# Optimization experiments

Hardware: AMD Instinct MI355X
Metric: run time of the kernel (lower is better)

The kernel has to match this reference:

```python
import jax, jax.numpy as jnp
import numpy as np

B, T, L, D, H = 8, 4, 512, 512, 8
HD = D // H
THR = 1.0
BETA = 0.5
EPS = 1e-5


def heaviside(x):
    return (x >= 0).astype(x.dtype)


def bn_eval(x, g, b, rm, rv):
    # BatchNorm1d in eval mode applied on the last dim
    return (x - rm) * (g * jax.lax.rsqrt(rv + EPS)) + b


def lif(x_btld):
    # snntorch Leaky(beta=0.5, threshold=1, reset='subtract'), mem init 0, scan over T
    xs = jnp.moveaxis(x_btld, 1, 0)  # (T,B,L,D)

    def step(mem, xt):
        reset = heaviside(mem - THR)          # reset from previous mem (detached in torch)
        mem = BETA * mem + xt - reset * THR
        spk = heaviside(mem - THR)
        return mem, spk

    _, spks = jax.lax.scan(step, jnp.zeros_like(xs[0]), xs)
    return jnp.moveaxis(spks, 0, 1)


def setup_inputs() -> dict:
    key = jax.random.key(0)
    ks = jax.random.split(key, 24)
    s = D ** -0.5
    inp = {
        "x": jax.random.normal(ks[0], (B, T, L, D), jnp.float32),
        "q_w": jax.random.normal(ks[1], (D, D), jnp.float32) * s,
        "q_g": jax.random.normal(ks[2], (D,), jnp.float32),
        "q_b": jax.random.normal(ks[3], (D,), jnp.float32),
        "q_rm": jax.random.normal(ks[4], (D,), jnp.float32),
        "q_rv": jax.random.uniform(ks[5], (D,), jnp.float32),
        "k_w": jax.random.normal(ks[6], (D, D), jnp.float32) * s,
        "k_g": jax.random.normal(ks[7], (D,), jnp.float32),
        "k_b": jax.random.normal(ks[8], (D,), jnp.float32),
        "k_rm": jax.random.normal(ks[9], (D,), jnp.float32),
        "k_rv": jax.random.uniform(ks[10], (D,), jnp.float32),
        "v_w": jax.random.normal(ks[11], (D, D), jnp.float32) * s,
        "v_g": jax.random.normal(ks[12], (D,), jnp.float32),
        "v_b": jax.random.normal(ks[13], (D,), jnp.float32),
        "v_rm": jax.random.normal(ks[14], (D,), jnp.float32),
        "v_rv": jax.random.uniform(ks[15], (D,), jnp.float32),
        "o_w": jax.random.normal(ks[16], (D, D), jnp.float32) * s,
        "o_bias": jax.random.normal(ks[17], (D,), jnp.float32),
        "o_g": jax.random.normal(ks[18], (D,), jnp.float32),
        "o_b": jax.random.normal(ks[19], (D,), jnp.float32),
        "o_rm": jax.random.normal(ks[20], (D,), jnp.float32),
        "o_rv": jax.random.uniform(ks[21], (D,), jnp.float32),
    }
    return inp


def reference(x, q_w, q_g, q_b, q_rm, q_rv, k_w, k_g, k_b, k_rm, k_rv,
              v_w, v_g, v_b, v_rm, v_rv, o_w, o_bias, o_g, o_b, o_rm, o_rv):
    scale = HD ** -0.5
    # Q path: linear -> BN -> LIF (binary {0,1})
    q = bn_eval(jnp.einsum('btld,ed->btle', x, q_w), q_g, q_b, q_rm, q_rv)
    q = lif(q)
    # K path: linear -> BN -> ReLU (continuous)
    k = jax.nn.relu(bn_eval(jnp.einsum('btld,ed->btle', x, k_w), k_g, k_b, k_rm, k_rv))
    # V path: linear -> BN -> ternary {-1,0,+1}
    v = bn_eval(jnp.einsum('btld,ed->btle', x, v_w), v_g, v_b, v_rm, v_rv)
    v = heaviside(v - THR) - heaviside(-v - THR)
    # split heads: (B,T,H,L,hd)
    sh = lambda a: a.reshape(B, T, L, H, HD).transpose(0, 1, 3, 2, 4)
    q, k, v = sh(q), sh(k), sh(v)
    attn = jnp.einsum('bthld,bthmd->bthlm', q, k) * scale
    out = jnp.einsum('bthlm,bthmd->bthld', attn, v)
    out = out.transpose(0, 1, 3, 2, 4).reshape(B, T, L, D)
    out = jnp.einsum('btld,ed->btle', out, o_w) + o_bias
    out = bn_eval(out, o_g, o_b, o_rm, o_rv)
    return lif(out)
```

## Files before the change

kernel.cpp:

```cpp
#include <hip/hip_runtime.h>
#include <math.h>
#include <stdint.h>

#define Bb 8
#define Tt 4
#define Ll 512
#define Dd 512
#define Hh 8
#define HDd 64
#define Mm (Bb*Tt*Ll)

typedef _Float16 f16;
typedef _Float16 f16x8 __attribute__((ext_vector_type(8)));
typedef _Float16 f16x4 __attribute__((ext_vector_type(4)));
typedef float f32x4 __attribute__((ext_vector_type(4)));

#define LO_SCALE 2048.0f
#define LO_INV   4.8828125e-4f

__device__ __forceinline__ void gload16(const void* g, void* l) {
  __builtin_amdgcn_global_load_lds(
      (const __attribute__((address_space(1))) unsigned int*)(uintptr_t)g,
      (__attribute__((address_space(3))) unsigned int*)(uintptr_t)l,
      16, 0, 0);
}

struct SplitArgs {
  const float* src[5];
  f16* hi[5];
  f16* lo[5];
};

__global__ void split_k(SplitArgs s) {
  int i = blockIdx.x * 256 + threadIdx.x;
  int seg, base;
  if (i < 1048576) { seg = 0; base = i; }
  else { int r = i - 1048576; seg = 1 + (r >> 15); base = r & 32767; }
  const float* sp = s.src[seg] + (size_t)base * 8;
  float4 v0 = *(const float4*)sp;
  float4 v1 = *(const float4*)(sp + 4);
  float a[8] = {v0.x, v0.y, v0.z, v0.w, v1.x, v1.y, v1.z, v1.w};
  f16x8 hv, lv;
  #pragma unroll
  for (int e = 0; e < 8; ++e) {
    f16 hh = (f16)a[e];
    hv[e] = hh;
    lv[e] = (f16)((a[e] - (float)hh) * LO_SCALE);
  }
  *(f16x8*)(s.hi[seg] + (size_t)base * 8) = hv;
  *(f16x8*)(s.lo[seg] + (size_t)base * 8) = lv;
}

struct GArgs {
  const f16 *Ah, *Al;
  const f16 *Wh0, *Wl0, *Wh1, *Wl1, *Wh2, *Wl2;
  const float *g0,*b0,*rm0,*rv0;
  const float *g1,*b1,*rm1,*rv1;
  const float *g2,*b2,*rm2,*rv2;
  const float* bias;
  f16*   oq;
  float* ok;
  f16*   ov;
  float* oo;
};

#define SMEM_BYTES 34048

template<int MODE>
__global__ __launch_bounds__(256, 2)
void gemm_f16(GArgs ar) {
  extern __shared__ __align__(16) char smem[];
  f16* Ah_s = (f16*)smem;
  f16* Al_s = (f16*)(smem + 8192);
  f16* Bh_s = (f16*)(smem + 16384);
  f16* Bl_s = (f16*)(smem + 24576);
  float (*TS)[133] = (float(*)[133])smem;

  const int tid = threadIdx.x;
  const int lane = tid & 63, wid = tid >> 6;
  const int bx = blockIdx.x, by = blockIdx.y;
  const int seg = (MODE == 0) ? (bx >> 2) : 0;
  const int lc0 = (MODE == 0) ? ((bx & 3) << 7) : (bx << 7);
  const int b = by >> 4, lc32 = by & 15;

  const f16* Wh = (seg == 0 ? ar.Wh0 : (seg == 1 ? ar.Wh1 : ar.Wh2));
  const f16* Wl = (seg == 0 ? ar.Wl0 : (seg == 1 ? ar.Wl1 : ar.Wl2));
  const float* gp  = (seg == 0 ? ar.g0  : (seg == 1 ? ar.g1  : ar.g2));
  const float* bp  = (seg == 0 ? ar.b0  : (seg == 1 ? ar.b1  : ar.b2));
  const float* rmp = (seg == 0 ? ar.rm0 : (seg == 1 ? ar.rm1 : ar.rm2));
  const float* rvp = (seg == 0 ? ar.rv0 : (seg == 1 ? ar.rv1 : ar.rv2));

  const int srow = lane >> 2, skc = lane & 3;
  const int fr = lane & 15, kg = lane >> 4;
  const int wmr = wid >> 1, wnc = wid & 1;

  f32x4 acc_h[4][4], acc_l[4][4];
  #pragma unroll
  for (int i = 0; i < 4; ++i)
    #pragma unroll
    for (int j = 0; j < 4; ++j) {
      acc_h[i][j] = (f32x4)0.0f;
      acc_l[i][j] = (f32x4)0.0f;
    }

  for (int k0 = 0; k0 < Dd; k0 += 32) {
    __syncthreads();
    #pragma unroll
    for (int i = 0; i < 2; ++i) {
      const int r = i * 64 + wid * 16 + srow;
      const int grow = (((b << 2) + (r >> 5)) << 9) + (lc32 << 5) + (r & 31);
      const size_t goA = (size_t)grow * Dd + k0 + skc * 8;
      const size_t goB = (size_t)(lc0 + r) * Dd + k0 + skc * 8;
      const int lbase = i * 2048 + wid * 512;
      gload16(ar.Ah + goA, Ah_s + lbase);
      gload16(ar.Al + goA, Al_s + lbase);
      gload16(Wh + goB, Bh_s + lbase);
      gload16(Wl + goB, Bl_s + lbase);
    }
    __syncthreads();

    f16x8 a_h[4], a_l[4], b_h[4], b_l[4];
    #pragma unroll
    for (int i = 0; i < 4; ++i) {
      const int ra = (wmr * 64 + i * 16 + fr) * 32 + kg * 8;
      a_h[i] = *(const f16x8*)&Ah_s[ra];
      a_l[i] = *(const f16x8*)&Al_s[ra];
      const int rb = (wnc * 64 + i * 16 + fr) * 32 + kg * 8;
      b_h[i] = *(const f16x8*)&Bh_s[rb];
      b_l[i] = *(const f16x8*)&Bl_s[rb];
    }
    #pragma unroll
    for (int i = 0; i < 4; ++i)
      #pragma unroll
      for (int j = 0; j < 4; ++j) {
        acc_h[i][j] = __builtin_amdgcn_mfma_f32_16x16x32_f16(a_h[i], b_h[j], acc_h[i][j], 0, 0, 0);
        acc_l[i][j] = __builtin_amdgcn_mfma_f32_16x16x32_f16(a_h[i], b_l[j], acc_l[i][j], 0, 0, 0);
        acc_l[i][j] = __builtin_amdgcn_mfma_f32_16x16x32_f16(a_l[i], b_h[j], acc_l[i][j], 0, 0, 0);
      }
  }

  float scl[4], shc[4];
  #pragma unroll
  for (int j = 0; j < 4; ++j) {
    const int c = lc0 + wnc * 64 + j * 16 + fr;
    double S = (double)gp[c] / sqrt((double)rvp[c] + 1e-5);
    double Sh = (double)bp[c] - (double)rmp[c] * S;
    if (MODE == 1) Sh += (double)ar.bias[c] * S;
    scl[j] = (float)S; shc[j] = (float)Sh;
  }

  if (MODE == 0 && seg != 0) {
    #pragma unroll
    for (int i = 0; i < 4; ++i)
      #pragma unroll
      for (int r = 0; r < 4; ++r) {
        const int tr = wmr * 64 + i * 16 + (kg << 2) + r;
        const int grow = (((b << 2) + (tr >> 5)) << 9) + (lc32 << 5) + (tr & 31);
        #pragma unroll
        for (int j = 0; j < 4; ++j) {
          const int col = lc0 + wnc * 64 + j * 16 + fr;
          float val = acc_h[i][j][r] + acc_l[i][j][r] * LO_INV;
          float y = val * scl[j] + shc[j];
          if (seg == 1) ar.ok[(size_t)grow * Dd + col] = fmaxf(y, 0.f);
          else ar.ov[(size_t)grow * Dd + col] =
                   (f16)((y >= 1.f ? 1.f : 0.f) - (-y >= 1.f ? 1.f : 0.f));
        }
      }
    return;
  }

  __syncthreads();
  #pragma unroll
  for (int half = 0; half < 2; ++half) {
    if (wnc == half) {
      #pragma unroll
      for (int i = 0; i < 4; ++i)
        #pragma unroll
        for (int j = 0; j < 4; ++j) {
          float4 yv;
          float* yp = &yv.x;
          #pragma unroll
          for (int r = 0; r < 4; ++r) {
            float val = acc_h[i][j][r] + acc_l[i][j][r] * LO_INV;
            yp[r] = val * scl[j] + shc[j];
          }
          *(float4*)&TS[j * 16 + fr][wmr * 64 + i * 16 + (kg << 2)] = yv;
        }
    }
    __syncthreads();
    const int cc4 = (tid & 15) << 2;
    #pragma unroll
    for (int rr = 0; rr < 2; ++rr) {
      const int rl = (tid >> 4) + (rr << 4);
      float mm[4] = {0.f, 0.f, 0.f, 0.f};
      #pragma unroll
      for (int t = 0; t < 4; ++t) {
        const int trow = t * 32 + rl;
        float sp[4];
        #pragma unroll
        for (int c = 0; c < 4; ++c) {
          float y = TS[cc4 + c][trow];
          float rst = (mm[c] >= 1.f) ? 1.f : 0.f;
          mm[c] = 0.5f * mm[c] + y - rst;
          sp[c] = (mm[c] >= 1.f) ? 1.f : 0.f;
        }
        const size_t go = ((size_t)((((b << 2) + t) << 9) + (lc32 << 5) + rl)) * Dd
                          + lc0 + (half << 6) + cc4;
        if (MODE == 0) {
          f16x4 s4;
          s4[0] = (f16)sp[0]; s4[1] = (f16)sp[1]; s4[2] = (f16)sp[2]; s4[3] = (f16)sp[3];
          *(f16x4*)(ar.oq + go) = s4;
        } else {
          *(float4*)(ar.oo + go) = make_float4(sp[0], sp[1], sp[2], sp[3]);
        }
      }
    }
    __syncthreads();
  }
}

__global__ __launch_bounds__(256)
void attn_g(const float* __restrict__ ks, const f16* __restrict__ vs,
            float* __restrict__ pG) {
  const int bt = blockIdx.x, h = blockIdx.y, c = blockIdx.z;
  const float* kp = ks + (size_t)bt * Ll * Dd + h * HDd;
  const f16* vp = vs + (size_t)bt * Ll * Dd + h * HDd;

  __shared__ float KS[64][68];
  __shared__ float VS[64][68];
  const int tid = threadIdx.x;
  const int te = tid & 15, td = tid >> 4;

  float gacc[4][4];
  #pragma unroll
  for (int i = 0; i < 4; ++i)
    #pragma unroll
    for (int j = 0; j < 4; ++j) gacc[i][j] = 0.f;

  for (int mt = 0; mt < 2; ++mt) {
    const int m0 = c * 128 + mt * 64;
    #pragma unroll
    for (int it = 0; it < 4; ++it) {
      int fidx = it * 256 + tid;
      int row = fidx >> 4, fq = fidx & 15;
      *(float4*)&KS[row][fq << 2] = *(const float4*)(kp + (size_t)(m0 + row) * Dd + (fq << 2));
    }
    #pragma unroll
    for (int it = 0; it < 2; ++it) {
      int fidx = it * 256 + tid;
      int row = fidx >> 3, c8 = fidx & 7;
      f16x8 hv = *(const f16x8*)(vp + (size_t)(m0 + row) * Dd + (c8 << 3));
      *(float4*)&VS[row][c8 << 3] = make_float4(hv[0], hv[1], hv[2], hv[3]);
      *(float4*)&VS[row][(c8 << 3) + 4] = make_float4(hv[4], hv[5], hv[6], hv[7]);
    }
    __syncthreads();
    #pragma unroll 4
    for (int mm = 0; mm < 64; ++mm) {
      float4 k4 = *(const float4*)&KS[mm][te << 2];
      float4 v4 = *(const float4*)&VS[mm][td << 2];
      const float kk[4] = {k4.x, k4.y, k4.z, k4.w};
      const float vv[4] = {v4.x, v4.y, v4.z, v4.w};
      #pragma unroll
      for (int i = 0; i < 4; ++i)
        #pragma unroll
        for (int j = 0; j < 4; ++j)
          gacc[i][j] = fmaf(kk[i], vv[j], gacc[i][j]);
    }
    __syncthreads();
  }
  float* out = pG + (((size_t)(bt * 8 + h) * 4 + c) << 12);
  #pragma unroll
  for (int i = 0; i < 4; ++i)
    *(float4*)&out[((te << 2) + i) * 64 + (td << 2)] =
        make_float4(gacc[i][0] * 0.125f, gacc[i][1] * 0.125f,
                    gacc[i][2] * 0.125f, gacc[i][3] * 0.125f);
}

__global__ __launch_bounds__(256)
void attn_o(const f16* __restrict__ qs, const float* __restrict__ pG,
            f16* __restrict__ ahi, f16* __restrict__ alo) {
  const int bt = blockIdx.x, h = blockIdx.y, lc = blockIdx.z;
  __shared__ float G[64][68];
  __shared__ float QS[64][68];
  const int tid = threadIdx.x;

  const float* pg = pG + (((size_t)(bt * 8 + h) * 4) << 12);
  #pragma unroll
  for (int rep = 0; rep < 4; ++rep) {
    int t4 = rep * 256 + tid;
    int e = t4 >> 4, dq = t4 & 15;
    int off = e * 64 + (dq << 2);
    float4 s0 = *(const float4*)(pg + off);
    float4 s1 = *(const float4*)(pg + 4096 + off);
    float4 s2 = *(const float4*)(pg + 8192 + off);
    float4 s3 = *(const float4*)(pg + 12288 + off);
    *(float4*)&G[e][dq << 2] = make_float4(s0.x + s1.x + s2.x + s3.x,
                                           s0.y + s1.y + s2.y + s3.y,
                                           s0.z + s1.z + s2.z + s3.z,
                                           s0.w + s1.w + s2.w + s3.w);
  }
  __syncthreads();

  const f16* qp = qs + (size_t)bt * Ll * Dd + h * HDd;
  const int lr = tid >> 2, dg = tid & 3;

  for (int l0 = 0; l0 < 128; l0 += 64) {
    #pragma unroll
    for (int it = 0; it < 2; ++it) {
      int fidx = it * 256 + tid;
      int row = fidx >> 3, c8 = fidx & 7;
      f16x8 hv = *(const f16x8*)(qp + (size_t)(lc * 128 + l0 + row) * Dd + (c8 << 3));
      *(float4*)&QS[row][c8 << 3] = make_float4(hv[0], hv[1], hv[2], hv[3]);
      *(float4*)&QS[row][(c8 << 3) + 4] = make_float4(hv[4], hv[5], hv[6], hv[7]);
    }
    __syncthreads();
    float oacc[16];
    #pragma unroll
    for (int j = 0; j < 16; ++j) oacc[j] = 0.f;
    for (int ee = 0; ee < 64; ++ee) {
      float qv = QS[lr][ee];
      #pragma unroll
      for (int jq = 0; jq < 4; ++jq) {
        float4 g4 = *(const float4*)&G[ee][(dg << 4) + (jq << 2)];
        oacc[jq * 4 + 0] = fmaf(qv, g4.x, oacc[jq * 4 + 0]);
        oacc[jq * 4 + 1] = fmaf(qv, g4.y, oacc[jq * 4 + 1]);
        oacc[jq * 4 + 2] = fmaf(qv, g4.z, oacc[jq * 4 + 2]);
        oacc[jq * 4 + 3] = fmaf(qv, g4.w, oacc[jq * 4 + 3]);
      }
    }
    f16x8 h0, l0v, h1, l1v;
    #pragma unroll
    for (int t = 0; t < 8; ++t) {
      float v = oacc[t];
      f16 hh = (f16)v;
      h0[t] = hh; l0v[t] = (f16)((v - (float)hh) * LO_SCALE);
      float v2 = oacc[8 + t];
      f16 hh2 = (f16)v2;
      h1[t] = hh2; l1v[t] = (f16)((v2 - (float)hh2) * LO_SCALE);
    }
    size_t ob = ((size_t)bt * Ll + lc * 128 + l0 + lr) * Dd + h * HDd + (dg << 4);
    *(f16x8*)(ahi + ob) = h0;
    *(f16x8*)(ahi + ob + 8) = h1;
    *(f16x8*)(alo + ob) = l0v;
    *(f16x8*)(alo + ob + 8) = l1v;
    __syncthreads();
  }
}

extern "C" void kernel_launch(void* const* d_in, const int* in_sizes, int n_in,
                              void* d_out, int out_size, void* d_ws, size_t ws_size,
                              hipStream_t stream) {
  const float* x    = (const float*)d_in[0];
  const float* q_w  = (const float*)d_in[1];
  const float* q_g  = (const float*)d_in[2];
  const float* q_b  = (const float*)d_in[3];
  const float* q_rm = (const float*)d_in[4];
  const float* q_rv = (const float*)d_in[5];
  const float* k_w  = (const float*)d_in[6];
  const float* k_g  = (const float*)d_in[7];
  const float* k_b  = (const float*)d_in[8];
  const float* k_rm = (const float*)d_in[9];
  const float* k_rv = (const float*)d_in[10];
  const float* v_w  = (const float*)d_in[11];
  const float* v_g  = (const float*)d_in[12];
  const float* v_b  = (const float*)d_in[13];
  const float* v_rm = (const float*)d_in[14];
  const float* v_rv = (const float*)d_in[15];
  const float* o_w  = (const float*)d_in[16];
  const float* o_bias = (const float*)d_in[17];
  const float* o_g  = (const float*)d_in[18];
  const float* o_b  = (const float*)d_in[19];
  const float* o_rm = (const float*)d_in[20];
  const float* o_rv = (const float*)d_in[21];

  char* wsb = (char*)d_ws;
  const size_t R16 = 16777216;
  f16*   xhi  = (f16*)wsb;
  f16*   xlo  = (f16*)(wsb + R16);
  f16*   qspk = (f16*)(wsb + 2 * R16);
  float* kbuf = (float*)(wsb + 3 * R16);
  f16*   vbuf = (f16*)(wsb + 5 * R16);
  float* pG   = (float*)(wsb + 6 * R16);
  f16*   wsp  = (f16*)(wsb + 7 * R16);
  f16* qwh = wsp;            f16* qwl = wsp + 262144;
  f16* kwh = wsp + 2*262144; f16* kwl = wsp + 3*262144;
  f16* vwh = wsp + 4*262144; f16* vwl = wsp + 5*262144;
  f16* owh = wsp + 6*262144; f16* owl = wsp + 7*262144;
  f16* ahi = xhi;
  f16* alo = xlo;

  SplitArgs sa;
  sa.src[0] = x;   sa.hi[0] = xhi; sa.lo[0] = xlo;
  sa.src[1] = q_w; sa.hi[1] = qwh; sa.lo[1] = qwl;
  sa.src[2] = k_w; sa.hi[2] = kwh; sa.lo[2] = kwl;
  sa.src[3] = v_w; sa.hi[3] = vwh; sa.lo[3] = vwl;
  sa.src[4] = o_w; sa.hi[4] = owh; sa.lo[4] = owl;
  split_k<<<4608, 256, 0, stream>>>(sa);

  GArgs a1;
  a1.Ah = xhi; a1.Al = xlo;
  a1.Wh0 = qwh; a1.Wl0 = qwl; a1.Wh1 = kwh; a1.Wl1 = kwl; a1.Wh2 = vwh; a1.Wl2 = vwl;
  a1.g0 = q_g; a1.b0 = q_b; a1.rm0 = q_rm; a1.rv0 = q_rv;
  a1.g1 = k_g; a1.b1 = k_b; a1.rm1 = k_rm; a1.rv1 = k_rv;
  a1.g2 = v_g; a1.b2 = v_b; a1.rm2 = v_rm; a1.rv2 = v_rv;
  a1.bias = nullptr;
  a1.oq = qspk; a1.ok = kbuf; a1.ov = vbuf; a1.oo = nullptr;
  gemm_f16<0><<<dim3(12, 128), 256, SMEM_BYTES, stream>>>(a1);

  attn_g<<<dim3(32, 8, 4), 256, 0, stream>>>(kbuf, vbuf, pG);
  attn_o<<<dim3(32, 8, 4), 256, 0, stream>>>(qspk, pG, ahi, alo);

  GArgs a2;
  a2.Ah = ahi; a2.Al = alo;
  a2.Wh0 = owh; a2.Wl0 = owl; a2.Wh1 = owh; a2.Wl1 = owl; a2.Wh2 = owh; a2.Wl2 = owl;
  a2.g0 = o_g; a2.b0 = o_b; a2.rm0 = o_rm; a2.rv0 = o_rv;
  a2.g1 = o_g; a2.b1 = o_b; a2.rm1 = o_rm; a2.rv1 = o_rv;
  a2.g2 = o_g; a2.b2 = o_b; a2.rm2 = o_rm; a2.rv2 = o_rv;
  a2.bias = o_bias;
  a2.oq = nullptr; a2.ok = nullptr; a2.ov = nullptr; a2.oo = (float*)d_out;
  gemm_f16<1><<<dim3(4, 128), 256, SMEM_BYTES, stream>>>(a2);
}
```

Before: 302.6 us.

## Double-buffer GEMM tiles, switch to 32x32 MFMA, swizzle LDS, remap block order

The split-f16 GEMM kernels now keep two LDS stages so the global-to-LDS loads of the next K slice run while MFMAs work on the current one. The inner product moves from 16x16x32 to 32x32x16 MFMA with f32x16 accumulators, and the LDS column index is XOR-swizzled to cut bank conflicts. Blocks are launched on a 1D grid and remapped in an interleaved order, likely to improve cache locality. LDS use grows to 64KB per block, which may limit occupancy, and the epilogue index mapping had to be rewritten for the new accumulator layout.

```diff
diff --git a/kernel.cpp b/kernel.cpp
--- a/kernel.cpp
+++ b/kernel.cpp
@@ -13,7 +13,7 @@
 typedef _Float16 f16;
 typedef _Float16 f16x8 __attribute__((ext_vector_type(8)));
 typedef _Float16 f16x4 __attribute__((ext_vector_type(4)));
-typedef float f32x4 __attribute__((ext_vector_type(4)));
+typedef float f32x16 __attribute__((ext_vector_type(16)));
 
 #define LO_SCALE 2048.0f
 #define LO_INV   4.8828125e-4f
@@ -64,21 +64,22 @@
   float* oo;
 };
 
-#define SMEM_BYTES 34048
+#define SMEM_BYTES 65536
 
 template<int MODE>
 __global__ __launch_bounds__(256, 2)
 void gemm_f16(GArgs ar) {
   extern __shared__ __align__(16) char smem[];
-  f16* Ah_s = (f16*)smem;
-  f16* Al_s = (f16*)(smem + 8192);
-  f16* Bh_s = (f16*)(smem + 16384);
-  f16* Bl_s = (f16*)(smem + 24576);
   float (*TS)[133] = (float(*)[133])smem;
 
   const int tid = threadIdx.x;
   const int lane = tid & 63, wid = tid >> 6;
-  const int bx = blockIdx.x, by = blockIdx.y;
+
+  const int bid = blockIdx.x;
+  int bx, by;
+  if (MODE == 0) { const int sw = (bid & 7) * 192 + (bid >> 3); bx = sw % 12; by = sw / 12; }
+  else           { const int sw = (bid & 7) * 64  + (bid >> 3); bx = sw & 3;  by = sw >> 2; }
+
   const int seg = (MODE == 0) ? (bx >> 2) : 0;
   const int lc0 = (MODE == 0) ? ((bx & 3) << 7) : (bx << 7);
   const int b = by >> 4, lc32 = by & 15;
@@ -90,102 +91,135 @@
   const float* rmp = (seg == 0 ? ar.rm0 : (seg == 1 ? ar.rm1 : ar.rm2));
   const float* rvp = (seg == 0 ? ar.rv0 : (seg == 1 ? ar.rv1 : ar.rv2));
 
-  const int srow = lane >> 2, skc = lane & 3;
-  const int fr = lane & 15, kg = lane >> 4;
+  const int sr = lane >> 2, skc = lane & 3;
+  const int skcs = skc ^ (sr & 3);
+  const int frow = lane & 31, khalf = lane >> 5;
   const int wmr = wid >> 1, wnc = wid & 1;
 
-  f32x4 acc_h[4][4], acc_l[4][4];
-  #pragma unroll
-  for (int i = 0; i < 4; ++i)
-    #pragma unroll
-    for (int j = 0; j < 4; ++j) {
-      acc_h[i][j] = (f32x4)0.0f;
-      acc_l[i][j] = (f32x4)0.0f;
-    }
-
-  for (int k0 = 0; k0 < Dd; k0 += 32) {
-    __syncthreads();
-    #pragma unroll
-    for (int i = 0; i < 2; ++i) {
-      const int r = i * 64 + wid * 16 + srow;
-      const int grow = (((b << 2) + (r >> 5)) << 9) + (lc32 << 5) + (r & 31);
-      const size_t goA = (size_t)grow * Dd + k0 + skc * 8;
-      const size_t goB = (size_t)(lc0 + r) * Dd + k0 + skc * 8;
-      const int lbase = i * 2048 + wid * 512;
-      gload16(ar.Ah + goA, Ah_s + lbase);
-      gload16(ar.Al + goA, Al_s + lbase);
-      gload16(Wh + goB, Bh_s + lbase);
-      gload16(Wl + goB, Bl_s + lbase);
-    }
-    __syncthreads();
-
-    f16x8 a_h[4], a_l[4], b_h[4], b_l[4];
-    #pragma unroll
-    for (int i = 0; i < 4; ++i) {
-      const int ra = (wmr * 64 + i * 16 + fr) * 32 + kg * 8;
-      a_h[i] = *(const f16x8*)&Ah_s[ra];
-      a_l[i] = *(const f16x8*)&Al_s[ra];
-      const int rb = (wnc * 64 + i * 16 + fr) * 32 + kg * 8;
-      b_h[i] = *(const f16x8*)&Bh_s[rb];
-      b_l[i] = *(const f16x8*)&Bl_s[rb];
-    }
-    #pragma unroll
-    for (int i = 0; i < 4; ++i)
-      #pragma unroll
-      for (int j = 0; j < 4; ++j) {
-        acc_h[i][j] = __builtin_amdgcn_mfma_f32_16x16x32_f16(a_h[i], b_h[j], acc_h[i][j], 0, 0, 0);
-        acc_l[i][j] = __builtin_amdgcn_mfma_f32_16x16x32_f16(a_h[i], b_l[j], acc_l[i][j], 0, 0, 0);
-        acc_l[i][j] = __builtin_amdgcn_mfma_f32_16x16x32_f16(a_l[i], b_h[j], acc_l[i][j], 0, 0, 0);
+  f32x16 acc_h[2][2], acc_l[2][2];
+  #pragma unroll
+  for (int i = 0; i < 2; ++i)
+    #pragma unroll
+    for (int j = 0; j < 2; ++j) {
+      acc_h[i][j] = (f32x16)0.0f;
+      acc_l[i][j] = (f32x16)0.0f;
+    }
+
+  #define STAGE(k0_, slot_)                                                        \
+    {                                                                              \
+      char* sb = smem + (slot_) * 32768;                                           \
+      _Pragma("unroll")                                                            \
+      for (int i = 0; i < 2; ++i) {                                                \
+        const int r = i * 64 + wid * 16 + sr;                                      \
+        const int growA = (((b << 2) + (r >> 5)) << 9) + (lc32 << 5) + (r & 31);   \
+        const size_t goA = (size_t)growA * Dd + (k0_) + skcs * 8;                  \
+        const size_t goB = (size_t)(lc0 + r) * Dd + (k0_) + skcs * 8;              \
+        const int lb = i * 2048 + wid * 512;                                       \
+        gload16(ar.Ah + goA, (f16*)sb + lb);                                       \
+        gload16(ar.Al + goA, (f16*)(sb + 8192) + lb);                              \
+        gload16(Wh + goB, (f16*)(sb + 16384) + lb);                                \
+        gload16(Wl + goB, (f16*)(sb + 24576) + lb);                                \
+      }                                                                            \
+    }
+
+  STAGE(0, 0);
+  __syncthreads();
+
+  for (int t = 0; t < 16; ++t) {
+    const int cur = t & 1;
+    const f16* Ahs = (const f16*)(smem + cur * 32768);
+    const f16* Als = Ahs + 4096;
+    const f16* Bhs = Ahs + 8192;
+    const f16* Bls = Ahs + 12288;
+
+    if (t < 15) STAGE((t + 1) * 32, cur ^ 1);
+
+    f16x8 ah[2][2], al[2][2], bh[2][2], bl[2][2];
+    #pragma unroll
+    for (int mi = 0; mi < 2; ++mi) {
+      const int r = wmr * 64 + mi * 32 + frow;
+      #pragma unroll
+      for (int ks = 0; ks < 2; ++ks) {
+        const int cin = (khalf + 2 * ks) ^ (lane & 3);
+        const int ad = r * 32 + cin * 8;
+        ah[mi][ks] = *(const f16x8*)&Ahs[ad];
+        al[mi][ks] = *(const f16x8*)&Als[ad];
       }
-  }
-
-  float scl[4], shc[4];
-  #pragma unroll
-  for (int j = 0; j < 4; ++j) {
-    const int c = lc0 + wnc * 64 + j * 16 + fr;
+    }
+    #pragma unroll
+    for (int nj = 0; nj < 2; ++nj) {
+      const int r = wnc * 64 + nj * 32 + frow;
+      #pragma unroll
+      for (int ks = 0; ks < 2; ++ks) {
+        const int cin = (khalf + 2 * ks) ^ (lane & 3);
+        const int ad = r * 32 + cin * 8;
+        bh[nj][ks] = *(const f16x8*)&Bhs[ad];
+        bl[nj][ks] = *(const f16x8*)&Bls[ad];
+      }
+    }
+    #pragma unroll
+    for (int ks = 0; ks < 2; ++ks)
+      #pragma unroll
+      for (int mi = 0; mi < 2; ++mi)
+        #pragma unroll
+        for (int nj = 0; nj < 2; ++nj) {
+          acc_h[mi][nj] = __builtin_amdgcn_mfma_f32_32x32x16_f16(ah[mi][ks], bh[nj][ks], acc_h[mi][nj], 0, 0, 0);
+          acc_l[mi][nj] = __builtin_amdgcn_mfma_f32_32x32x16_f16(ah[mi][ks], bl[nj][ks], acc_l[mi][nj], 0, 0, 0);
+          acc_l[mi][nj] = __builtin_amdgcn_mfma_f32_32x32x16_f16(al[mi][ks], bh[nj][ks], acc_l[mi][nj], 0, 0, 0);
+        }
+    __syncthreads();
+  }
+  #undef STAGE
+
+  float scl[2], shc[2];
+  #pragma unroll
+  for (int nj = 0; nj < 2; ++nj) {
+    const int c = lc0 + wnc * 64 + nj * 32 + frow;
     double S = (double)gp[c] / sqrt((double)rvp[c] + 1e-5);
     double Sh = (double)bp[c] - (double)rmp[c] * S;
     if (MODE == 1) Sh += (double)ar.bias[c] * S;
-    scl[j] = (float)S; shc[j] = (float)Sh;
+    scl[nj] = (float)S; shc[nj] = (float)Sh;
   }
 
   if (MODE == 0 && seg != 0) {
     #pragma unroll
-    for (int i = 0; i < 4; ++i)
-      #pragma unroll
-      for (int r = 0; r < 4; ++r) {
-        const int tr = wmr * 64 + i * 16 + (kg << 2) + r;
-        const int grow = (((b << 2) + (tr >> 5)) << 9) + (lc32 << 5) + (tr & 31);
+    for (int mi = 0; mi < 2; ++mi)
+      #pragma unroll
+      for (int nj = 0; nj < 2; ++nj)
         #pragma unroll
-        for (int j = 0; j < 4; ++j) {
-          const int col = lc0 + wnc * 64 + j * 16 + fr;
-          float val = acc_h[i][j][r] + acc_l[i][j][r] * LO_INV;
-          float y = val * scl[j] + shc[j];
+        for (int r = 0; r < 16; ++r) {
+          const int row32 = (r & 3) + 8 * (r >> 2) + 4 * khalf;
+          const int tr = wmr * 64 + mi * 32 + row32;
+          const int grow = (((b << 2) + (tr >> 5)) << 9) + (lc32 << 5) + (tr & 31);
+          const int col = lc0 + wnc * 64 + nj * 32 + frow;
+          float val = acc_h[mi][nj][r] + acc_l[mi][nj][r] * LO_INV;
+          float y = val * scl[nj] + shc[nj];
           if (seg == 1) ar.ok[(size_t)grow * Dd + col] = fmaxf(y, 0.f);
           else ar.ov[(size_t)grow * Dd + col] =
                    (f16)((y >= 1.f ? 1.f : 0.f) - (-y >= 1.f ? 1.f : 0.f));
         }
-      }
     return;
   }
 
-  __syncthreads();
   #pragma unroll
   for (int half = 0; half < 2; ++half) {
     if (wnc == half) {
       #pragma unroll
-      for (int i = 0; i < 4; ++i)
+      for (int mi = 0; mi < 2; ++mi)
         #pragma unroll
-        for (int j = 0; j < 4; ++j) {
-          float4 yv;
-          float* yp = &yv.x;
+        for (int nj = 0; nj < 2; ++nj)
           #pragma unroll
-          for (int r = 0; r < 4; ++r) {
-            float val = acc_h[i][j][r] + acc_l[i][j][r] * LO_INV;
-            yp[r] = val * scl[j] + shc[j];
+          for (int q = 0; q < 4; ++q) {
+            float4 yv;
+            float* yp = &yv.x;
+            #pragma unroll
+            for (int rr = 0; rr < 4; ++rr) {
+              const int r = q * 4 + rr;
+              float val = acc_h[mi][nj][r] + acc_l[mi][nj][r] * LO_INV;
+              yp[rr] = val * scl[nj] + shc[nj];
+            }
+            *(float4*)&TS[nj * 32 + frow][wmr * 64 + mi * 32 + 8 * q + 4 * khalf] = yv;
           }
-          *(float4*)&TS[j * 16 + fr][wmr * 64 + i * 16 + (kg << 2)] = yv;
-        }
     }
     __syncthreads();
     const int cc4 = (tid & 15) << 2;
@@ -405,7 +439,7 @@
   a1.g2 = v_g; a1.b2 = v_b; a1.rm2 = v_rm; a1.rv2 = v_rv;
   a1.bias = nullptr;
   a1.oq = qspk; a1.ok = kbuf; a1.ov = vbuf; a1.oo = nullptr;
-  gemm_f16<0><<<dim3(12, 128), 256, SMEM_BYTES, stream>>>(a1);
+  gemm_f16<0><<<1536, 256, SMEM_BYTES, stream>>>(a1);
 
   attn_g<<<dim3(32, 8, 4), 256, 0, stream>>>(kbuf, vbuf, pG);
   attn_o<<<dim3(32, 8, 4), 256, 0, stream>>>(qspk, pG, ahi, alo);
@@ -418,5 +452,5 @@
   a2.g2 = o_g; a2.b2 = o_b; a2.rm2 = o_rm; a2.rv2 = o_rv;
   a2.bias = o_bias;
   a2.oq = nullptr; a2.ok = nullptr; a2.ov = nullptr; a2.oo = (float*)d_out;
-  gemm_f16<1><<<dim3(4, 128), 256, SMEM_BYTES, stream>>>(a2);
-}
+  gemm_f16<1><<<512, 256, SMEM_BYTES, stream>>>(a2);
+}
```

Result: no change. 307.2 us (+1.5%).
